# Optimization experiments

Hardware: AMD Instinct MI355X
Metric: run time of the kernel (lower is better)

## Reference

```python
import jax, jax.numpy as jnp
import numpy as np

HIDDEN, KEY_DIM, VALUE_DIM = 1024, 64, 64
B, T = 4, 4096


def setup_inputs() -> dict:
    key = jax.random.key(0)
    ks = jax.random.split(key, 9)
    s = 0.02
    return {
        "y_all": jax.random.normal(ks[0], (B, T, HIDDEN), dtype=jnp.float32),
        # torch nn.Linear weights: (out_features, in_features)
        "Wq": jax.random.normal(ks[1], (KEY_DIM, HIDDEN), dtype=jnp.float32) * s,
        "bq": jax.random.normal(ks[2], (KEY_DIM,), dtype=jnp.float32) * s,
        "Wk": jax.random.normal(ks[3], (KEY_DIM, HIDDEN), dtype=jnp.float32) * s,
        "bk": jax.random.normal(ks[4], (KEY_DIM,), dtype=jnp.float32) * s,
        "Wv": jax.random.normal(ks[5], (VALUE_DIM, HIDDEN), dtype=jnp.float32) * s,
        "bv": jax.random.normal(ks[6], (VALUE_DIM,), dtype=jnp.float32) * s,
        "Wo": jax.random.normal(ks[7], (HIDDEN, VALUE_DIM), dtype=jnp.float32) * s,
        "bo": jax.random.normal(ks[8], (HIDDEN,), dtype=jnp.float32) * s,
    }


def reference(y_all, Wq, bq, Wk, bk, Wv, bv, Wo, bo):
    # The original per-timestep loop is exactly causal self-attention:
    # query at position i attends over positions 0..i.
    q = jnp.einsum("bth,kh->btk", y_all, Wq) + bq          # (B,T,Dk)
    k = jnp.einsum("bth,kh->btk", y_all, Wk) + bk          # (B,T,Dk)
    v = jnp.einsum("bth,vh->btv", y_all, Wv) + bv          # (B,T,Dv)
    scale = jnp.asarray(KEY_DIM, q.dtype) ** 0.5
    scores = jnp.einsum("bqk,btk->bqt", q / scale, k)      # (B,T,T)
    t = scores.shape[-1]
    causal = jnp.tril(jnp.ones((t, t), dtype=bool))
    scores = jnp.where(causal, scores, jnp.asarray(-jnp.inf, scores.dtype))
    weights = jax.nn.softmax(scores, axis=-1)
    ctx = jnp.einsum("bqt,btv->bqv", weights, v)           # (B,T,Dv)
    out = jnp.einsum("bqv,hv->bqh", ctx, Wo) + bo          # (B,T,H)
    return out
```

## Files before the change

### kernel.cpp

```cpp
#include <hip/hip_runtime.h>


typedef __attribute__((ext_vector_type(4)))  float f32x4;
typedef __attribute__((ext_vector_type(16))) float f32x16;
typedef __attribute__((ext_vector_type(8)))  short s16x8;
typedef __attribute__((ext_vector_type(4)))  short s16x4;

#define DEV static __device__ __forceinline__

static constexpr int TT = 4096;
static constexpr int HH = 1024;
static constexpr int DD = 64;
static constexpr float MNEG = -3.0e38f;

DEV unsigned short f2bf(float f) {
  union { float f; unsigned int u; } v; v.f = f;
  unsigned int r = v.u + 0x7FFFu + ((v.u >> 16) & 1u);
  return (unsigned short)(r >> 16);
}

DEV unsigned int pk2(float lo, float hi) {
  return (unsigned int)f2bf(lo) | ((unsigned int)f2bf(hi) << 16);
}

DEV s16x8 mk8(unsigned int w0, unsigned int w1, unsigned int w2, unsigned int w3) {
  union { unsigned int u[4]; s16x8 v; } c;
  c.u[0] = w0; c.u[1] = w1; c.u[2] = w2; c.u[3] = w3; return c.v;
}

DEV int swzA(int row) { return ((row & 7) << 4); }
DEV int swzK(int row) { return ((row & 7) << 4) ^ ((row & 8) << 3); }

__global__ void prep_kernel(const float* __restrict__ Wq, const float* __restrict__ Wk,
                            const float* __restrict__ Wv, const float* __restrict__ Wo,
                            unsigned short* __restrict__ Wall,
                            unsigned short* __restrict__ Wo_b)
{
  int i = blockIdx.x * blockDim.x + threadIdx.x;
  int stride = gridDim.x * blockDim.x;
  const int n1 = 64 * HH;
  for (int idx = i; idx < 3 * n1; idx += stride) {
    float v = idx < n1 ? Wq[idx] : (idx < 2 * n1 ? Wk[idx - n1] : Wv[idx - 2 * n1]);
    Wall[idx] = f2bf(v);
  }
  for (int idx = i; idx < HH * DD; idx += stride) {
    int hcol = idx >> 6, d = idx & 63;
    size_t off = (size_t)(hcol >> 4) * 1024 + (d >> 5) * 512 + (hcol & 15) * 32
               + ((d >> 3) & 3) * 8 + (d & 7);
    Wo_b[off] = f2bf(Wo[idx]);
  }
}

__global__ __launch_bounds__(256) void qkv_kernel(
    const float* __restrict__ y, const unsigned short* __restrict__ Wall,
    const float* __restrict__ bq, const float* __restrict__ bk,
    const float* __restrict__ bv,
    unsigned short* __restrict__ q_ws, unsigned short* __restrict__ k_ws,
    unsigned short* __restrict__ vT_ws)
{
  __shared__ unsigned short ylds[2][64 * 64];
  __shared__ unsigned short wlds[2][192 * 64];
  const int t = threadIdx.x;
  const int w = t >> 6, lane = t & 63, g = lane >> 4, c = lane & 15;
  const int row0 = blockIdx.x * 64;
  const int yrow = t >> 2, ycol0 = (t & 3) * 16;

  f32x4 acc[12];
#pragma unroll
  for (int i = 0; i < 12; ++i)
#pragma unroll
    for (int e = 0; e < 4; ++e) acc[i][e] = 0.0f;

  f32x4 yr[4];
  s16x8 wr[6];

  auto load_tiles = [&](int kb) {
    const float* src = y + (size_t)(row0 + yrow) * HH + kb * 64 + ycol0;
    yr[0] = *(const f32x4*)(src);
    yr[1] = *(const f32x4*)(src + 4);
    yr[2] = *(const f32x4*)(src + 8);
    yr[3] = *(const f32x4*)(src + 12);
#pragma unroll
    for (int ii = 0; ii < 6; ++ii) {
      int ch = t + ii * 256;
      int rw = ch >> 3, c0 = (ch & 7) * 8;
      wr[ii] = *(const s16x8*)(Wall + (size_t)rw * HH + kb * 64 + c0);
    }
  };
  auto write_tiles = [&](int buf) {
    s16x8 h0, h1;
#pragma unroll
    for (int e = 0; e < 4; ++e) {
      h0[e]     = (short)f2bf(yr[0][e]);
      h0[e + 4] = (short)f2bf(yr[1][e]);
      h1[e]     = (short)f2bf(yr[2][e]);
      h1[e + 4] = (short)f2bf(yr[3][e]);
    }
    int byte0 = yrow * 128 + ycol0 * 2;
    *(s16x8*)((char*)ylds[buf] + (byte0 ^ swzA(yrow)))        = h0;
    *(s16x8*)((char*)ylds[buf] + ((byte0 + 16) ^ swzA(yrow))) = h1;
#pragma unroll
    for (int ii = 0; ii < 6; ++ii) {
      int ch = t + ii * 256;
      int rw = ch >> 3, c0 = (ch & 7) * 8;
      int byte = rw * 128 + c0 * 2;
      *(s16x8*)((char*)wlds[buf] + (byte ^ swzA(rw))) = wr[ii];
    }
  };

  load_tiles(0);
  write_tiles(0);
  __syncthreads();
  for (int kb = 0; kb < 16; ++kb) {
    int buf = kb & 1;
    if (kb < 15) load_tiles(kb + 1);
#pragma unroll
    for (int kk = 0; kk < 2; ++kk) {
      int r = 16 * w + c;
      s16x8 a = *(const s16x8*)((char*)ylds[buf] +
                  ((r * 128 + (kk * 32 + 8 * g) * 2) ^ swzA(r)));
#pragma unroll
      for (int nt = 0; nt < 12; ++nt) {
        int rb = 16 * nt + c;
        s16x8 b = *(const s16x8*)((char*)wlds[buf] +
                    ((rb * 128 + (kk * 32 + 8 * g) * 2) ^ swzA(rb)));
        acc[nt] = __builtin_amdgcn_mfma_f32_16x16x32_bf16(a, b, acc[nt], 0, 0, 0);
      }
    }
    __syncthreads();
    if (kb < 15) { write_tiles((kb + 1) & 1); __syncthreads(); }
  }

  const float qsc = 1.4426950408889634f / 8.0f;
  const int bb = row0 >> 12;
  const int tb = row0 & 4095;
#pragma unroll
  for (int nt = 0; nt < 12; ++nt) {
    int sec = nt >> 2;
    int dcol = (nt & 3) * 16 + c;
    float bias = sec == 0 ? bq[dcol] : (sec == 1 ? bk[dcol] : bv[dcol]);
    if (sec == 2) {
      s16x4 pv;
#pragma unroll
      for (int i = 0; i < 4; ++i) pv[i] = (short)f2bf(acc[nt][i] + bias);
      int t0 = tb + 16 * w + 4 * g;
      size_t off = (size_t)bb * (DD * TT) + (size_t)(t0 >> 6) * 4096
                 + (dcol >> 5) * 2048 + w * 512 + (dcol & 31) * 16 + (t0 & 15);
      *(s16x4*)(vT_ws + off) = pv;
    } else {
      unsigned short* dst = sec == 0 ? q_ws : k_ws;
      int kk = nt & 3;
#pragma unroll
      for (int i = 0; i < 4; ++i) {
        int t_in = tb + 16 * w + 4 * g + i;
        float val = acc[nt][i] + bias;
        if (sec == 0) val *= qsc;
        size_t off = (size_t)bb * (TT * DD) + (size_t)(t_in >> 5) * 2048
                   + kk * 512 + (t_in & 31) * 16 + c;
        dst[off] = f2bf(val);
      }
    }
  }
}

__global__ __launch_bounds__(512, 2) void attn_kernel(
    const unsigned short* __restrict__ q_ws, const unsigned short* __restrict__ k_ws,
    const unsigned short* __restrict__ vT_ws, const unsigned short* __restrict__ Wo_b,
    const float* __restrict__ bo, float* __restrict__ out)
{
  __shared__ float obuf[2][3 * 2048];
  __shared__ float mstat[2][3 * 128];
  __shared__ unsigned short clds[2][32 * 64];
  const int t = threadIdx.x, wv = t >> 6, lane = t & 63;
  const int sub = wv >> 2, wv4 = wv & 3;
  const int qcol = lane & 31, h = lane >> 5;
  const int b = blockIdx.x & 3;
  const int u = blockIdx.x >> 2;
  const int j32 = sub ? (127 - u) : u;
  const int q0 = j32 * 32;
  const int L = j32 >> 1;
  const size_t base  = (size_t)b * TT * DD;
  const size_t vbase = (size_t)b * DD * TT;
  const int g = lane >> 4, c = lane & 15;
  const int lchunk = (lane & 31) * 16 + (lane >> 5) * 8;

  s16x8 qf[4];
  {
    const unsigned short* qp = q_ws + base + (size_t)j32 * 2048;
#pragma unroll
    for (int kk = 0; kk < 4; ++kk) qf[kk] = *(const s16x8*)(qp + kk * 512 + lchunk);
  }
  f32x16 o[2];
#pragma unroll
  for (int mt = 0; mt < 2; ++mt)
#pragma unroll
    for (int rg = 0; rg < 16; ++rg) o[mt][rg] = 0.0f;
  float m_run = MNEG, l_run = 0.0f;

  for (int kt = wv4; kt <= L; kt += 4) {
    const int kv0 = kt * 64;
    s16x8 kf[2][4];
#pragma unroll
    for (int mt = 0; mt < 2; ++mt)
#pragma unroll
      for (int kk = 0; kk < 4; ++kk)
        kf[mt][kk] = *(const s16x8*)(k_ws + base +
                       (size_t)(2 * kt + mt) * 2048 + kk * 512 + lchunk);
    f32x16 s[2];
#pragma unroll
    for (int mt = 0; mt < 2; ++mt)
#pragma unroll
      for (int rg = 0; rg < 16; ++rg) s[mt][rg] = 0.0f;
    __builtin_amdgcn_s_setprio(1);
#pragma unroll
    for (int kk = 0; kk < 4; ++kk)
#pragma unroll
      for (int mt = 0; mt < 2; ++mt)
        s[mt] = __builtin_amdgcn_mfma_f32_32x32x16_bf16(kf[mt][kk], qf[kk], s[mt], 0, 0, 0);
    __builtin_amdgcn_s_setprio(0);
    s16x8 vf[2][4];
#pragma unroll
    for (int mt = 0; mt < 2; ++mt)
#pragma unroll
      for (int ks = 0; ks < 4; ++ks)
        vf[mt][ks] = *(const s16x8*)(vT_ws + vbase +
                       (size_t)kt * 4096 + mt * 2048 + ks * 512 + lchunk);
    if (kt == L) {
      int qq = q0 + qcol;
#pragma unroll
      for (int mt = 0; mt < 2; ++mt)
#pragma unroll
        for (int rg = 0; rg < 16; ++rg) {
          int kvabs = kv0 + 32 * mt + (rg & 3) + 8 * (rg >> 2) + 4 * h;
          if (kvabs > qq) s[mt][rg] = MNEG;
        }
    }
    float mx[16];
#pragma unroll
    for (int e = 0; e < 16; ++e) mx[e] = fmaxf(s[0][e], s[1][e]);
#pragma unroll
    for (int st = 8; st >= 1; st >>= 1)
#pragma unroll
      for (int e = 0; e < 8; ++e) if (e < st) mx[e] = fmaxf(mx[e], mx[e + st]);
    float pm = fmaxf(mx[0], __shfl_xor(mx[0], 32));
    float m_new = fmaxf(m_run, pm);
    float alpha = exp2f(m_run - m_new);
#pragma unroll
    for (int mt = 0; mt < 2; ++mt)
#pragma unroll
      for (int rg = 0; rg < 16; ++rg) s[mt][rg] = exp2f(s[mt][rg] - m_new);
    float sm[16];
#pragma unroll
    for (int e = 0; e < 16; ++e) sm[e] = s[0][e] + s[1][e];
#pragma unroll
    for (int st = 8; st >= 1; st >>= 1)
#pragma unroll
      for (int e = 0; e < 8; ++e) if (e < st) sm[e] += sm[e + st];
    float rowsum = sm[0] + __shfl_xor(sm[0], 32);
    l_run = l_run * alpha + rowsum;
    m_run = m_new;
#pragma unroll
    for (int mt = 0; mt < 2; ++mt)
#pragma unroll
      for (int rg = 0; rg < 16; ++rg) o[mt][rg] *= alpha;
    s16x8 pf[4];
#pragma unroll
    for (int mt = 0; mt < 2; ++mt) {
      unsigned int a0 = pk2(s[mt][0],  s[mt][1]);
      unsigned int a1 = pk2(s[mt][2],  s[mt][3]);
      unsigned int b0 = pk2(s[mt][4],  s[mt][5]);
      unsigned int b1 = pk2(s[mt][6],  s[mt][7]);
      unsigned int c0 = pk2(s[mt][8],  s[mt][9]);
      unsigned int c1 = pk2(s[mt][10], s[mt][11]);
      unsigned int d0 = pk2(s[mt][12], s[mt][13]);
      unsigned int d1 = pk2(s[mt][14], s[mt][15]);
      unsigned int t0 = __shfl_xor(h ? a0 : b0, 32);
      unsigned int t1 = __shfl_xor(h ? a1 : b1, 32);
      unsigned int t2 = __shfl_xor(h ? c0 : d0, 32);
      unsigned int t3 = __shfl_xor(h ? c1 : d1, 32);
      pf[2 * mt]     = mk8(h ? t0 : a0, h ? t1 : a1, h ? b0 : t0, h ? b1 : t1);
      pf[2 * mt + 1] = mk8(h ? t2 : c0, h ? t3 : c1, h ? d0 : t2, h ? d1 : t3);
    }
    __builtin_amdgcn_s_setprio(1);
#pragma unroll
    for (int ks = 0; ks < 4; ++ks)
#pragma unroll
      for (int mt = 0; mt < 2; ++mt)
        o[mt] = __builtin_amdgcn_mfma_f32_32x32x16_bf16(vf[mt][ks], pf[ks], o[mt], 0, 0, 0);
    __builtin_amdgcn_s_setprio(0);
  }

  if (wv4 != 0) {
    float* ob = &obuf[sub][(wv4 - 1) * 2048];
#pragma unroll
    for (int mt = 0; mt < 2; ++mt)
#pragma unroll
      for (int rg = 0; rg < 16; ++rg)
        ob[(mt * 16 + rg) * 64 + lane] = o[mt][rg];
    mstat[sub][(wv4 - 1) * 128 + lane] = m_run;
    mstat[sub][(wv4 - 1) * 128 + 64 + lane] = l_run;
  }
  __syncthreads();
  if (wv4 == 0) {
    float mB[3], lB[3];
    float mS = m_run;
#pragma unroll
    for (int i = 0; i < 3; ++i) {
      mB[i] = mstat[sub][i * 128 + lane];
      lB[i] = mstat[sub][i * 128 + 64 + lane];
      mS = fmaxf(mS, mB[i]);
    }
    float f0 = exp2f(m_run - mS);
    float fi[3];
    float l_tot = l_run * f0;
#pragma unroll
    for (int i = 0; i < 3; ++i) { fi[i] = exp2f(mB[i] - mS); l_tot += lB[i] * fi[i]; }
    float inv = 1.0f / l_tot;
#pragma unroll
    for (int mt = 0; mt < 2; ++mt) {
#pragma unroll
      for (int rgq = 0; rgq < 4; ++rgq) {
        s16x4 pb;
#pragma unroll
        for (int e = 0; e < 4; ++e) {
          int rg = 4 * rgq + e;
          float val = o[mt][rg] * f0;
#pragma unroll
          for (int i = 0; i < 3; ++i)
            val += obuf[sub][i * 2048 + (mt * 16 + rg) * 64 + lane] * fi[i];
          pb[e] = (short)f2bf(val * inv);
        }
        int d0 = 32 * mt + 8 * rgq + 4 * h;
        int byte = qcol * 128 + d0 * 2;
        *(s16x4*)((char*)clds[sub] + (byte ^ swzK(qcol))) = pb;
      }
    }
  }
  __syncthreads();

  s16x8 afr[2][2];
#pragma unroll
  for (int mt = 0; mt < 2; ++mt)
#pragma unroll
    for (int kk = 0; kk < 2; ++kk) {
      int ra = 16 * mt + c;
      afr[mt][kk] = *(const s16x8*)((char*)clds[sub] +
                      ((ra * 128 + (32 * kk + 8 * g) * 2) ^ swzK(ra)));
    }
  const int wchunk = (lane & 15) * 32 + (lane >> 4) * 8;
  const size_t orow0 = (size_t)(b * TT + q0);
#pragma unroll 4
  for (int nt = 0; nt < 16; ++nt) {
    int col = wv4 * 256 + 16 * nt + c;
    s16x8 bfr[2];
#pragma unroll
    for (int kk = 0; kk < 2; ++kk)
      bfr[kk] = *(const s16x8*)(Wo_b + (size_t)(wv4 * 16 + nt) * 1024
                                + kk * 512 + wchunk);
    f32x4 acc4[2];
#pragma unroll
    for (int mt = 0; mt < 2; ++mt)
#pragma unroll
      for (int e = 0; e < 4; ++e) acc4[mt][e] = 0.0f;
#pragma unroll
    for (int kk = 0; kk < 2; ++kk)
#pragma unroll
      for (int mt = 0; mt < 2; ++mt)
        acc4[mt] = __builtin_amdgcn_mfma_f32_16x16x32_bf16(afr[mt][kk], bfr[kk],
                                                           acc4[mt], 0, 0, 0);
    float bias = bo[col];
#pragma unroll
    for (int mt = 0; mt < 2; ++mt)
#pragma unroll
      for (int i = 0; i < 4; ++i) {
        size_t row = orow0 + 16 * mt + 4 * g + i;
        out[row * HH + col] = acc4[mt][i] + bias;
      }
  }
}

extern "C" void kernel_launch(void* const* d_in, const int* in_sizes, int n_in,
                              void* d_out, int out_size, void* d_ws, size_t ws_size,
                              hipStream_t stream)
{
  const float* y  = (const float*)d_in[0];
  const float* Wq = (const float*)d_in[1];
  const float* bq = (const float*)d_in[2];
  const float* Wk = (const float*)d_in[3];
  const float* bk = (const float*)d_in[4];
  const float* Wv = (const float*)d_in[5];
  const float* bv = (const float*)d_in[6];
  const float* Wo = (const float*)d_in[7];
  const float* bo = (const float*)d_in[8];
  float* out = (float*)d_out;
  char* ws = (char*)d_ws;
  unsigned short* Wall  = (unsigned short*)(ws);
  unsigned short* Wo_b  = (unsigned short*)(ws + 393216);
  unsigned short* q_ws  = (unsigned short*)(ws + 524288);
  unsigned short* k_ws  = (unsigned short*)(ws + 524288 + 2097152);
  unsigned short* vT_ws = (unsigned short*)(ws + 524288 + 2 * 2097152);

  prep_kernel<<<dim3(256), dim3(256), 0, stream>>>(Wq, Wk, Wv, Wo, Wall, Wo_b);
  qkv_kernel<<<dim3(256), dim3(256), 0, stream>>>(y, Wall, bq, bk, bv, q_ws, k_ws, vT_ws);
  attn_kernel<<<dim3(256), dim3(512), 0, stream>>>(q_ws, k_ws, vT_ws, Wo_b, bo, out);
}
```

Baseline: 68.24 us.

## Retile QKV projection, widen attention to 16 waves, add lazy softmax rescale

The QKV kernel now uses 32-row tiles over 512 blocks, with waves split across output columns. Its results are staged through LDS so Q, K and V^T can be written to global memory with coalesced 16-byte stores. The attention kernel doubles to 1024 threads, so each query tile's KV range is split across 8 waves instead of 4. The partial outputs are stored as bf16 in one shared buffer to fit in LDS. The online softmax skips the rescale whenever the new max exceeds the running max by at most 8 in log2 units. This cuts exp and multiply work, but risks precision loss from the bf16 partials and from values up to 2^8 above the stale max.

```diff
diff --git a/kernel.cpp b/kernel.cpp
--- a/kernel.cpp
+++ b/kernel.cpp
@@ -17,6 +17,11 @@
   union { float f; unsigned int u; } v; v.f = f;
   unsigned int r = v.u + 0x7FFFu + ((v.u >> 16) & 1u);
   return (unsigned short)(r >> 16);
+}
+
+DEV float bf2f(unsigned short u) {
+  union { unsigned int u; float f; } v; v.u = ((unsigned int)u) << 16;
+  return v.f;
 }
 
 DEV unsigned int pk2(float lo, float hi) {
@@ -51,35 +56,37 @@
   }
 }
 
-__global__ __launch_bounds__(256) void qkv_kernel(
+__global__ __launch_bounds__(256, 2) void qkv_kernel(
     const float* __restrict__ y, const unsigned short* __restrict__ Wall,
     const float* __restrict__ bq, const float* __restrict__ bk,
     const float* __restrict__ bv,
     unsigned short* __restrict__ q_ws, unsigned short* __restrict__ k_ws,
     unsigned short* __restrict__ vT_ws)
 {
-  __shared__ unsigned short ylds[2][64 * 64];
+  __shared__ unsigned short ylds[2][32 * 64];
   __shared__ unsigned short wlds[2][192 * 64];
   const int t = threadIdx.x;
-  const int w = t >> 6, lane = t & 63, g = lane >> 4, c = lane & 15;
-  const int row0 = blockIdx.x * 64;
-  const int yrow = t >> 2, ycol0 = (t & 3) * 16;
-
-  f32x4 acc[12];
-#pragma unroll
-  for (int i = 0; i < 12; ++i)
-#pragma unroll
-    for (int e = 0; e < 4; ++e) acc[i][e] = 0.0f;
-
-  f32x4 yr[4];
+  const int wv = t >> 6, lane = t & 63, g = lane >> 4, c = lane & 15;
+  const int row0 = blockIdx.x * 32;
+  const int bb = row0 >> 12;
+  const int tb = row0 & 4095;
+  const int yrow = t >> 3, ycol0 = (t & 7) * 8;
+
+  f32x4 acc[2][3];
+#pragma unroll
+  for (int m = 0; m < 2; ++m)
+#pragma unroll
+    for (int i = 0; i < 3; ++i)
+#pragma unroll
+      for (int e = 0; e < 4; ++e) acc[m][i][e] = 0.0f;
+
+  f32x4 yr[2];
   s16x8 wr[6];
 
   auto load_tiles = [&](int kb) {
     const float* src = y + (size_t)(row0 + yrow) * HH + kb * 64 + ycol0;
     yr[0] = *(const f32x4*)(src);
     yr[1] = *(const f32x4*)(src + 4);
-    yr[2] = *(const f32x4*)(src + 8);
-    yr[3] = *(const f32x4*)(src + 12);
 #pragma unroll
     for (int ii = 0; ii < 6; ++ii) {
       int ch = t + ii * 256;
@@ -88,17 +95,14 @@
     }
   };
   auto write_tiles = [&](int buf) {
-    s16x8 h0, h1;
+    s16x8 h0;
 #pragma unroll
     for (int e = 0; e < 4; ++e) {
       h0[e]     = (short)f2bf(yr[0][e]);
       h0[e + 4] = (short)f2bf(yr[1][e]);
-      h1[e]     = (short)f2bf(yr[2][e]);
-      h1[e + 4] = (short)f2bf(yr[3][e]);
     }
     int byte0 = yrow * 128 + ycol0 * 2;
-    *(s16x8*)((char*)ylds[buf] + (byte0 ^ swzA(yrow)))        = h0;
-    *(s16x8*)((char*)ylds[buf] + ((byte0 + 16) ^ swzA(yrow))) = h1;
+    *(s16x8*)((char*)ylds[buf] + (byte0 ^ swzA(yrow))) = h0;
 #pragma unroll
     for (int ii = 0; ii < 6; ++ii) {
       int ch = t + ii * 256;
@@ -116,63 +120,77 @@
     if (kb < 15) load_tiles(kb + 1);
 #pragma unroll
     for (int kk = 0; kk < 2; ++kk) {
-      int r = 16 * w + c;
-      s16x8 a = *(const s16x8*)((char*)ylds[buf] +
-                  ((r * 128 + (kk * 32 + 8 * g) * 2) ^ swzA(r)));
-#pragma unroll
-      for (int nt = 0; nt < 12; ++nt) {
-        int rb = 16 * nt + c;
-        s16x8 b = *(const s16x8*)((char*)wlds[buf] +
-                    ((rb * 128 + (kk * 32 + 8 * g) * 2) ^ swzA(rb)));
-        acc[nt] = __builtin_amdgcn_mfma_f32_16x16x32_bf16(a, b, acc[nt], 0, 0, 0);
-      }
+      s16x8 a[2], bfr[3];
+#pragma unroll
+      for (int m = 0; m < 2; ++m) {
+        int ra = 16 * m + c;
+        a[m] = *(const s16x8*)((char*)ylds[buf] +
+                 ((ra * 128 + (kk * 32 + 8 * g) * 2) ^ swzA(ra)));
+      }
+#pragma unroll
+      for (int i = 0; i < 3; ++i) {
+        int rb = 16 * (3 * wv + i) + c;
+        bfr[i] = *(const s16x8*)((char*)wlds[buf] +
+                   ((rb * 128 + (kk * 32 + 8 * g) * 2) ^ swzA(rb)));
+      }
+#pragma unroll
+      for (int m = 0; m < 2; ++m)
+#pragma unroll
+        for (int i = 0; i < 3; ++i)
+          acc[m][i] = __builtin_amdgcn_mfma_f32_16x16x32_bf16(a[m], bfr[i], acc[m][i], 0, 0, 0);
     }
     __syncthreads();
     if (kb < 15) { write_tiles((kb + 1) & 1); __syncthreads(); }
   }
 
+  unsigned short* elds = &wlds[0][0];
   const float qsc = 1.4426950408889634f / 8.0f;
-  const int bb = row0 >> 12;
-  const int tb = row0 & 4095;
-#pragma unroll
-  for (int nt = 0; nt < 12; ++nt) {
-    int sec = nt >> 2;
-    int dcol = (nt & 3) * 16 + c;
-    float bias = sec == 0 ? bq[dcol] : (sec == 1 ? bk[dcol] : bv[dcol]);
-    if (sec == 2) {
-      s16x4 pv;
-#pragma unroll
-      for (int i = 0; i < 4; ++i) pv[i] = (short)f2bf(acc[nt][i] + bias);
-      int t0 = tb + 16 * w + 4 * g;
-      size_t off = (size_t)bb * (DD * TT) + (size_t)(t0 >> 6) * 4096
-                 + (dcol >> 5) * 2048 + w * 512 + (dcol & 31) * 16 + (t0 & 15);
-      *(s16x4*)(vT_ws + off) = pv;
-    } else {
-      unsigned short* dst = sec == 0 ? q_ws : k_ws;
-      int kk = nt & 3;
-#pragma unroll
-      for (int i = 0; i < 4; ++i) {
-        int t_in = tb + 16 * w + 4 * g + i;
-        float val = acc[nt][i] + bias;
+#pragma unroll
+  for (int m = 0; m < 2; ++m)
+#pragma unroll
+    for (int i = 0; i < 3; ++i) {
+      int nt = 3 * wv + i;
+      int sec = nt >> 2;
+      int dcol = (nt & 3) * 16 + c;
+      float bias = sec == 0 ? bq[dcol] : (sec == 1 ? bk[dcol] : bv[dcol]);
+#pragma unroll
+      for (int i2 = 0; i2 < 4; ++i2) {
+        int rl = 16 * m + 4 * g + i2;
+        float val = acc[m][i][i2] + bias;
         if (sec == 0) val *= qsc;
-        size_t off = (size_t)bb * (TT * DD) + (size_t)(t_in >> 5) * 2048
-                   + kk * 512 + (t_in & 31) * 16 + c;
-        dst[off] = f2bf(val);
-      }
-    }
-  }
-}
-
-__global__ __launch_bounds__(512, 2) void attn_kernel(
+        if (sec < 2) elds[sec * 2048 + rl * 64 + dcol] = f2bf(val);
+        else         elds[4096 + dcol * 32 + rl]       = f2bf(val);
+      }
+    }
+  __syncthreads();
+  {
+    int trow = t >> 3, d0 = (t & 7) * 8;
+    s16x8 vq = *(const s16x8*)(elds + trow * 64 + d0);
+    s16x8 vk = *(const s16x8*)(elds + 2048 + trow * 64 + d0);
+    size_t offqk = (size_t)bb * (TT * DD) + (size_t)(tb >> 5) * 2048
+                 + (d0 >> 4) * 512 + trow * 16 + (d0 & 15);
+    *(s16x8*)(q_ws + offqk) = vq;
+    *(s16x8*)(k_ws + offqk) = vk;
+    int d = t >> 2, tq = (t & 3) * 8;
+    s16x8 vvv = *(const s16x8*)(elds + 4096 + d * 32 + tq);
+    int tg = tb + tq;
+    size_t offv = (size_t)bb * (DD * TT) + (size_t)(tg >> 6) * 4096
+                + (d >> 5) * 2048 + ((tg >> 4) & 3) * 512 + (d & 31) * 16 + (tg & 15);
+    *(s16x8*)(vT_ws + offv) = vvv;
+  }
+}
+
+__global__ __launch_bounds__(1024) void attn_kernel(
     const unsigned short* __restrict__ q_ws, const unsigned short* __restrict__ k_ws,
     const unsigned short* __restrict__ vT_ws, const unsigned short* __restrict__ Wo_b,
     const float* __restrict__ bo, float* __restrict__ out)
 {
-  __shared__ float obuf[2][3 * 2048];
-  __shared__ float mstat[2][3 * 128];
-  __shared__ unsigned short clds[2][32 * 64];
+  __shared__ char smem[64512];
+  unsigned short* obuf = (unsigned short*)smem;
+  float* mstat = (float*)(smem + 57344);
+  unsigned short* clds = (unsigned short*)smem;
   const int t = threadIdx.x, wv = t >> 6, lane = t & 63;
-  const int sub = wv >> 2, wv4 = wv & 3;
+  const int sub = wv >> 3, wp = wv & 7;
   const int qcol = lane & 31, h = lane >> 5;
   const int b = blockIdx.x & 3;
   const int u = blockIdx.x >> 2;
@@ -197,7 +215,7 @@
     for (int rg = 0; rg < 16; ++rg) o[mt][rg] = 0.0f;
   float m_run = MNEG, l_run = 0.0f;
 
-  for (int kt = wv4; kt <= L; kt += 4) {
+  for (int kt = wp; kt <= L; kt += 8) {
     const int kv0 = kt * 64;
     s16x8 kf[2][4];
 #pragma unroll
@@ -243,8 +261,19 @@
 #pragma unroll
       for (int e = 0; e < 8; ++e) if (e < st) mx[e] = fmaxf(mx[e], mx[e + st]);
     float pm = fmaxf(mx[0], __shfl_xor(mx[0], 32));
-    float m_new = fmaxf(m_run, pm);
-    float alpha = exp2f(m_run - m_new);
+    float m_new;
+    if (__all(pm - m_run <= 8.0f)) {
+      m_new = m_run;
+    } else {
+      m_new = fmaxf(m_run, pm);
+      float alpha = exp2f(m_run - m_new);
+      l_run *= alpha;
+#pragma unroll
+      for (int mt = 0; mt < 2; ++mt)
+#pragma unroll
+        for (int rg = 0; rg < 16; ++rg) o[mt][rg] *= alpha;
+      m_run = m_new;
+    }
 #pragma unroll
     for (int mt = 0; mt < 2; ++mt)
 #pragma unroll
@@ -257,12 +286,7 @@
 #pragma unroll
       for (int e = 0; e < 8; ++e) if (e < st) sm[e] += sm[e + st];
     float rowsum = sm[0] + __shfl_xor(sm[0], 32);
-    l_run = l_run * alpha + rowsum;
-    m_run = m_new;
-#pragma unroll
-    for (int mt = 0; mt < 2; ++mt)
-#pragma unroll
-      for (int rg = 0; rg < 16; ++rg) o[mt][rg] *= alpha;
+    l_run += rowsum;
     s16x8 pf[4];
 #pragma unroll
     for (int mt = 0; mt < 2; ++mt) {
@@ -290,49 +314,55 @@
     __builtin_amdgcn_s_setprio(0);
   }
 
-  if (wv4 != 0) {
-    float* ob = &obuf[sub][(wv4 - 1) * 2048];
+  if (wp != 0) {
+    unsigned short* ob = obuf + (sub * 7 + wp - 1) * 2048;
 #pragma unroll
     for (int mt = 0; mt < 2; ++mt)
 #pragma unroll
       for (int rg = 0; rg < 16; ++rg)
-        ob[(mt * 16 + rg) * 64 + lane] = o[mt][rg];
-    mstat[sub][(wv4 - 1) * 128 + lane] = m_run;
-    mstat[sub][(wv4 - 1) * 128 + 64 + lane] = l_run;
+        ob[(mt * 16 + rg) * 64 + lane] = f2bf(o[mt][rg]);
+    mstat[(sub * 7 + wp - 1) * 128 + lane] = m_run;
+    mstat[(sub * 7 + wp - 1) * 128 + 64 + lane] = l_run;
   }
   __syncthreads();
-  if (wv4 == 0) {
-    float mB[3], lB[3];
+  if (wp == 0) {
+    float mB[7], lB[7];
     float mS = m_run;
 #pragma unroll
-    for (int i = 0; i < 3; ++i) {
-      mB[i] = mstat[sub][i * 128 + lane];
-      lB[i] = mstat[sub][i * 128 + 64 + lane];
+    for (int i = 0; i < 7; ++i) {
+      mB[i] = mstat[(sub * 7 + i) * 128 + lane];
+      lB[i] = mstat[(sub * 7 + i) * 128 + 64 + lane];
       mS = fmaxf(mS, mB[i]);
     }
     float f0 = exp2f(m_run - mS);
-    float fi[3];
+    float fi[7];
     float l_tot = l_run * f0;
 #pragma unroll
-    for (int i = 0; i < 3; ++i) { fi[i] = exp2f(mB[i] - mS); l_tot += lB[i] * fi[i]; }
+    for (int i = 0; i < 7; ++i) { fi[i] = exp2f(mB[i] - mS); l_tot += lB[i] * fi[i]; }
     float inv = 1.0f / l_tot;
+#pragma unroll
+    for (int mt = 0; mt < 2; ++mt)
+#pragma unroll
+      for (int rg = 0; rg < 16; ++rg) {
+        float val = o[mt][rg] * f0;
+#pragma unroll
+        for (int i = 0; i < 7; ++i)
+          val += bf2f(obuf[(sub * 7 + i) * 2048 + (mt * 16 + rg) * 64 + lane]) * fi[i];
+        o[mt][rg] = val * inv;
+      }
+  }
+  __syncthreads();
+  if (wp == 0) {
 #pragma unroll
     for (int mt = 0; mt < 2; ++mt) {
 #pragma unroll
       for (int rgq = 0; rgq < 4; ++rgq) {
         s16x4 pb;
 #pragma unroll
-        for (int e = 0; e < 4; ++e) {
-          int rg = 4 * rgq + e;
-          float val = o[mt][rg] * f0;
-#pragma unroll
-          for (int i = 0; i < 3; ++i)
-            val += obuf[sub][i * 2048 + (mt * 16 + rg) * 64 + lane] * fi[i];
-          pb[e] = (short)f2bf(val * inv);
-        }
+        for (int e = 0; e < 4; ++e) pb[e] = (short)f2bf(o[mt][4 * rgq + e]);
         int d0 = 32 * mt + 8 * rgq + 4 * h;
         int byte = qcol * 128 + d0 * 2;
-        *(s16x4*)((char*)clds[sub] + (byte ^ swzK(qcol))) = pb;
+        *(s16x4*)((char*)clds + sub * 4096 + (byte ^ swzK(qcol))) = pb;
       }
     }
   }
@@ -344,19 +374,19 @@
 #pragma unroll
     for (int kk = 0; kk < 2; ++kk) {
       int ra = 16 * mt + c;
-      afr[mt][kk] = *(const s16x8*)((char*)clds[sub] +
+      afr[mt][kk] = *(const s16x8*)((char*)clds + sub * 4096 +
                       ((ra * 128 + (32 * kk + 8 * g) * 2) ^ swzK(ra)));
     }
   const int wchunk = (lane & 15) * 32 + (lane >> 4) * 8;
   const size_t orow0 = (size_t)(b * TT + q0);
 #pragma unroll 4
-  for (int nt = 0; nt < 16; ++nt) {
-    int col = wv4 * 256 + 16 * nt + c;
+  for (int nt = 0; nt < 8; ++nt) {
+    int nt16 = wp * 8 + nt;
+    int col = nt16 * 16 + c;
     s16x8 bfr[2];
 #pragma unroll
     for (int kk = 0; kk < 2; ++kk)
-      bfr[kk] = *(const s16x8*)(Wo_b + (size_t)(wv4 * 16 + nt) * 1024
-                                + kk * 512 + wchunk);
+      bfr[kk] = *(const s16x8*)(Wo_b + (size_t)nt16 * 1024 + kk * 512 + wchunk);
     f32x4 acc4[2];
 #pragma unroll
     for (int mt = 0; mt < 2; ++mt)
@@ -401,6 +431,6 @@
   unsigned short* vT_ws = (unsigned short*)(ws + 524288 + 2 * 2097152);
 
   prep_kernel<<<dim3(256), dim3(256), 0, stream>>>(Wq, Wk, Wv, Wo, Wall, Wo_b);
-  qkv_kernel<<<dim3(256), dim3(256), 0, stream>>>(y, Wall, bq, bk, bv, q_ws, k_ws, vT_ws);
-  attn_kernel<<<dim3(256), dim3(512), 0, stream>>>(q_ws, k_ws, vT_ws, Wo_b, bo, out);
-}
+  qkv_kernel<<<dim3(512), dim3(256), 0, stream>>>(y, Wall, bq, bk, bv, q_ws, k_ws, vT_ws);
+  attn_kernel<<<dim3(256), dim3(1024), 0, stream>>>(q_ws, k_ws, vT_ws, Wo_b, bo, out);
+}
```

After: 73.41 us. 7.6% more time.
